# Kernel tuning notes

Hardware: AMD Instinct MI355X
Metric: run time of the kernel (lower is better)

The kernel has to match this reference:

```python
import jax, jax.numpy as jnp
import numpy as np

EPS = 1e-5  # nn.LayerNorm default eps
N_LAYERS, N, D_IN, H, D_OUT, NH = 4, 2048, 512, 1024, 256, 16


def setup_inputs() -> dict:
    key = jax.random.key(0)
    ks = jax.random.split(key, 8)
    s = lambda k, shape: (jax.random.normal(k, shape, jnp.float32) * 0.02)
    return {
        "x": jax.random.normal(ks[0], (N, D_IN), jnp.float32),
        "W1": s(ks[1], (H, D_IN)), "b1": jnp.zeros((H,), jnp.float32),
        # per-layer MHA params, stacked on a leading layer axis
        "Wqkv": s(ks[2], (N_LAYERS, 3 * H, H)), "bqkv": jnp.zeros((N_LAYERS, 3 * H), jnp.float32),
        "Wo": s(ks[3], (N_LAYERS, H, H)), "bo": jnp.zeros((N_LAYERS, H), jnp.float32),
        "ln_g": jnp.ones((N_LAYERS, H), jnp.float32), "ln_b": jnp.zeros((N_LAYERS, H), jnp.float32),
        "W2": s(ks[4], (D_OUT, H)), "b2": jnp.zeros((D_OUT,), jnp.float32),
        "g_out": jnp.ones((D_OUT,), jnp.float32), "b_out": jnp.zeros((D_OUT,), jnp.float32),
        "num_heads": NH,
    }


def layer_norm(x, g, b):
    m = jnp.mean(x, axis=-1, keepdims=True)
    v = jnp.mean(jnp.square(x - m), axis=-1, keepdims=True)
    return (x - m) * jax.lax.rsqrt(v + EPS) * g + b


def mha(x, Wqkv, bqkv, Wo, bo, nh):
    # x: [N, H]; attention is over the N axis (torch MHA with batch_first=False, batch=1)
    n, h = x.shape
    hd = h // nh
    qkv = x @ Wqkv.T + bqkv                      # [N, 3H]
    q, k, v = jnp.split(qkv, 3, axis=-1)
    q = q.reshape(n, nh, hd).transpose(1, 0, 2)  # [nh, N, hd]
    k = k.reshape(n, nh, hd).transpose(1, 0, 2)
    v = v.reshape(n, nh, hd).transpose(1, 0, 2)
    scale = jnp.float32(1.0 / np.sqrt(hd))
    scores = jnp.einsum('hnd,hmd->hnm', q, k) * scale  # [nh, N, N]
    attn = jax.nn.softmax(scores, axis=-1)
    out = jnp.einsum('hnm,hmd->hnd', attn, v)          # [nh, N, hd]
    out = out.transpose(1, 0, 2).reshape(n, h)
    return out @ Wo.T + bo


def reference(x, W1, b1, Wqkv, bqkv, Wo, bo, ln_g, ln_b, W2, b2, g_out, b_out, num_heads):
    h = jax.nn.relu(x @ W1.T + b1)  # dropout is identity in eval mode
    for i in range(Wqkv.shape[0]):
        a = mha(h, Wqkv[i], bqkv[i], Wo[i], bo[i], num_heads)
        h = layer_norm(a + h, ln_g[i], ln_b[i])
    y = jax.nn.relu(h @ W2.T + b2)
    return layer_norm(y, g_out, b_out)
```

## Files before the change

### kernel.cpp

```cpp
#include <hip/hip_runtime.h>

typedef __attribute__((ext_vector_type(8))) short short8;
typedef __attribute__((ext_vector_type(4))) float f32x4;
typedef __attribute__((ext_vector_type(16))) float f32x16;
typedef __attribute__((ext_vector_type(4))) float float4v;
typedef __attribute__((ext_vector_type(4))) unsigned short ushort4v;
typedef __attribute__((ext_vector_type(4))) unsigned int uint4v;
typedef __attribute__((ext_vector_type(2))) unsigned int uint2v;

#define MFMA16(a, b, c) __builtin_amdgcn_mfma_f32_16x16x32_bf16((a), (b), (c), 0, 0, 0)
#define MFMA32(a, b, c) __builtin_amdgcn_mfma_f32_32x32x16_bf16((a), (b), (c), 0, 0, 0)
#define GLOAD_LDS16(g, s)                                                         \
  __builtin_amdgcn_global_load_lds((const __attribute__((address_space(1))) void*)(g), \
                                   (__attribute__((address_space(3))) void*)(s), 16, 0, 0)
#define EXP2(x) __builtin_amdgcn_exp2f(x)

__device__ __forceinline__ unsigned short f2bf(float f) {
  unsigned u = __builtin_bit_cast(unsigned, f);
  u += 0x7fffu + ((u >> 16) & 1u);
  return (unsigned short)(u >> 16);
}

__device__ __forceinline__ unsigned cvtpk(float lo, float hi) {
  unsigned r;
  asm("v_cvt_pk_bf16_f32 %0, %1, %2" : "=v"(r) : "v"(lo), "v"(hi));
  return r;
}

__device__ __forceinline__ void swap32(unsigned& a, unsigned& b) {
  asm volatile("v_permlane32_swap_b32 %0, %1" : "+v"(a), "+v"(b));
}

__device__ __forceinline__ float bflo(unsigned u) {
  return __builtin_bit_cast(float, u << 16);
}
__device__ __forceinline__ float bfhi(unsigned u) {
  return __builtin_bit_cast(float, u & 0xffff0000u);
}

struct CvtArgs {
  const float* s[5];
  unsigned short* d[5];
  int off[6];
};

__global__ __launch_bounds__(256) void cvt_multi(CvtArgs a, int ntot4) {
  int i4 = blockIdx.x * 256 + threadIdx.x;
  const int stride = gridDim.x * 256;
  for (; i4 < ntot4; i4 += stride) {
    const int idx = i4 * 4;
    int s = 0;
#pragma unroll
    for (int k = 0; k < 4; ++k) s += (idx >= a.off[k + 1]) ? 1 : 0;
    const int local = idx - a.off[s];
    float4v v = *(const float4v*)(a.s[s] + local);
    ushort4v o;
    o.x = f2bf(v.x); o.y = f2bf(v.y); o.z = f2bf(v.z); o.w = f2bf(v.w);
    *(ushort4v*)(a.d[s] + local) = o;
  }
}

template <int BM, int BN, bool RELU, bool RES, bool OUTF, bool OUTB, bool OUTT>
__global__ __launch_bounds__(256) void gemm_bt(const unsigned short* __restrict__ A,
                                               const unsigned short* __restrict__ B,
                                               const float* __restrict__ bias,
                                               const float* __restrict__ res,
                                               float* __restrict__ outF,
                                               unsigned short* __restrict__ outB,
                                               unsigned short* __restrict__ outT,
                                               int tcol0, int ldt,
                                               int M, int N, int K) {
  __shared__ __align__(16) unsigned short As[2][BM * 32];
  __shared__ __align__(16) unsigned short Bs[2][BN * 32];
  constexpr int MI = BM / 32, MJ = BN / 32, CA = BM / 64, CB = BN / 64;
  const int tid = threadIdx.x;
  const int w = tid >> 6, lane = tid & 63;
  const int l15 = lane & 15, l4 = lane >> 4;

  const int nwg = gridDim.x;
  const int wg = (blockIdx.x & 7) * (nwg >> 3) + (blockIdx.x >> 3);
  const int nbx = N / BN;
  const int rowBase = (wg / nbx) * BM;
  const int colBase = (wg % nbx) * BN;
  const int wm = w >> 1, wn = w & 1;

  f32x4 acc[MI][MJ] = {};

  auto stage = [&](int buf, int k0) {
#pragma unroll
    for (int i = 0; i < CA; ++i) {
      const int c = i * 256 + tid;
      GLOAD_LDS16(A + (size_t)(rowBase + (c >> 2)) * K + k0 + ((c & 3) << 3),
                  As[buf] + i * 2048 + w * 512);
    }
#pragma unroll
    for (int i = 0; i < CB; ++i) {
      const int c = i * 256 + tid;
      GLOAD_LDS16(B + (size_t)(colBase + (c >> 2)) * K + k0 + ((c & 3) << 3),
                  Bs[buf] + i * 2048 + w * 512);
    }
  };

  stage(0, 0);
  __syncthreads();

  int p = 0;
  for (int k0 = 0; k0 < K; k0 += 32) {
    if (k0 + 32 < K) stage(p ^ 1, k0 + 32);

    short8 af[MI], bf[MJ];
#pragma unroll
    for (int f = 0; f < MI; ++f)
      af[f] = *(const short8*)(As[p] + (wm * (BM / 2) + f * 16 + l15) * 32 + l4 * 8);
#pragma unroll
    for (int f = 0; f < MJ; ++f)
      bf[f] = *(const short8*)(Bs[p] + (wn * (BN / 2) + f * 16 + l15) * 32 + l4 * 8);
#pragma unroll
    for (int i = 0; i < MI; ++i)
#pragma unroll
      for (int j = 0; j < MJ; ++j)
        acc[i][j] = MFMA16(af[i], bf[j], acc[i][j]);

    __syncthreads();
    p ^= 1;
  }

#pragma unroll
  for (int i = 0; i < MI; ++i) {
    const int row0 = rowBase + wm * (BM / 2) + i * 16 + l4 * 4;
#pragma unroll
    for (int j = 0; j < MJ; ++j) {
      const int col = colBase + wn * (BN / 2) + j * 16 + l15;
      const float bv = bias[col];
      float vv[4];
#pragma unroll
      for (int e = 0; e < 4; ++e) {
        float v = acc[i][j][e] + bv;
        if constexpr (RELU) v = fmaxf(v, 0.f);
        if constexpr (RES) v += res[(size_t)(row0 + e) * N + col];
        vv[e] = v;
        if constexpr (OUTF) outF[(size_t)(row0 + e) * N + col] = v;
        if constexpr (OUTB) outB[(size_t)(row0 + e) * N + col] = f2bf(v);
      }
      if constexpr (OUTT) {
        if (col >= tcol0) {
          ushort4v t;
          t.x = f2bf(vv[0]); t.y = f2bf(vv[1]); t.z = f2bf(vv[2]); t.w = f2bf(vv[3]);
          *(ushort4v*)(outT + (size_t)(col - tcol0) * ldt + row0) = t;
        }
      }
    }
  }
}

__global__ __launch_bounds__(256, 3) void flash_attn4(const unsigned short* __restrict__ qkv,
                                                      const unsigned short* __restrict__ vt,
                                                      unsigned short* __restrict__ Op0,
                                                      unsigned short* __restrict__ OpR,
                                                      float* __restrict__ Ml,
                                                      float* __restrict__ Ll,
                                                      int Nseq) {
  __shared__ __align__(16) unsigned short Ks[2][64 * 64];
  __shared__ __align__(16) unsigned short Vs[2][64 * 64];
  const int tid = threadIdx.x, w = tid >> 6, lane = tid & 63;
  const int l31 = lane & 31, l2h = lane >> 5, l7 = l31 & 7;
  const float CSC = 0.18033688011112042f;

  const int b = blockIdx.x;
  const int head = (b & 7) * 2 + ((b >> 3) & 1);
  const int s = (b >> 4) & 3;
  const int qb = b >> 6;
  const int q0w = qb * 128 + w * 32;

  const unsigned short* Qp = qkv + head * 64;
  const unsigned short* Kp = qkv + 1024 + head * 64;
  const unsigned short* Vtp = vt + (size_t)head * 64 * Nseq;

  short8 qf[4];
#pragma unroll
  for (int ka = 0; ka < 4; ++ka)
    qf[ka] = *(const short8*)(Qp + (size_t)(q0w + l31) * 3072 + ka * 16 + l2h * 8);

  f32x16 OT0 = {}, OT1 = {};
  float m = -1e30f, ls = 0.f;

  const int sr = tid >> 3, su = tid & 7;
  const int sOffA = sr * 64 + ((su ^ (sr & 7)) * 8);
  const int sOffB = sOffA + 32 * 64;

  const int kt0 = s * (Nseq >> 2);
  const int NIT = Nseq >> 8;

  short8 k0 = *(const short8*)(Kp + (size_t)(kt0 + sr) * 3072 + su * 8);
  short8 k1 = *(const short8*)(Kp + (size_t)(kt0 + sr + 32) * 3072 + su * 8);
  short8 v0 = *(const short8*)(Vtp + (size_t)sr * Nseq + kt0 + su * 8);
  short8 v1 = *(const short8*)(Vtp + (size_t)(sr + 32) * Nseq + kt0 + su * 8);
  *(short8*)(Ks[0] + sOffA) = k0;
  *(short8*)(Ks[0] + sOffB) = k1;
  *(short8*)(Vs[0] + sOffA) = v0;
  *(short8*)(Vs[0] + sOffB) = v1;
  __syncthreads();

  int p = 0;
  for (int it = 0; it < NIT; ++it) {
    const bool more = (it + 1) < NIT;
    if (more) {
      const int ktn = kt0 + (it + 1) * 64;
      k0 = *(const short8*)(Kp + (size_t)(ktn + sr) * 3072 + su * 8);
      k1 = *(const short8*)(Kp + (size_t)(ktn + sr + 32) * 3072 + su * 8);
      v0 = *(const short8*)(Vtp + (size_t)sr * Nseq + ktn + su * 8);
      v1 = *(const short8*)(Vtp + (size_t)(sr + 32) * Nseq + ktn + su * 8);
    }
    const unsigned short* KS = Ks[p];
    const unsigned short* VS = Vs[p];

    f32x16 S0 = {}, S1 = {};
    __builtin_amdgcn_s_setprio(1);
#pragma unroll
    for (int ka = 0; ka < 4; ++ka) {
      const int un = ((ka * 2 + l2h) ^ l7) * 8;
      const short8 a0 = *(const short8*)(KS + l31 * 64 + un);
      const short8 a1 = *(const short8*)(KS + (32 + l31) * 64 + un);
      S0 = MFMA32(a0, qf[ka], S0);
      S1 = MFMA32(a1, qf[ka], S1);
    }
    __builtin_amdgcn_s_setprio(0);

    float pm = S0[0];
#pragma unroll
    for (int r = 1; r < 16; ++r) pm = fmaxf(pm, S0[r]);
#pragma unroll
    for (int r = 0; r < 16; ++r) pm = fmaxf(pm, S1[r]);
    pm = fmaxf(pm, __shfl_xor(pm, 32));
    pm *= CSC;

    if (__any(pm > m + 8.f)) {
      const float mn = fmaxf(m, pm);
      const float fac = EXP2(m - mn);
      m = mn;
      ls *= fac;
#pragma unroll
      for (int r = 0; r < 16; ++r) { OT0[r] *= fac; OT1[r] *= fac; }
    }

    float rs = 0.f;
    unsigned W0[4][2], W1[4][2];
#pragma unroll
    for (int g = 0; g < 4; ++g) {
      const float a0 = EXP2(fmaf(S0[4 * g + 0], CSC, -m));
      const float a1 = EXP2(fmaf(S0[4 * g + 1], CSC, -m));
      const float a2 = EXP2(fmaf(S0[4 * g + 2], CSC, -m));
      const float a3 = EXP2(fmaf(S0[4 * g + 3], CSC, -m));
      const float b0 = EXP2(fmaf(S1[4 * g + 0], CSC, -m));
      const float b1 = EXP2(fmaf(S1[4 * g + 1], CSC, -m));
      const float b2 = EXP2(fmaf(S1[4 * g + 2], CSC, -m));
      const float b3 = EXP2(fmaf(S1[4 * g + 3], CSC, -m));
      rs += ((a0 + a1) + (a2 + a3)) + ((b0 + b1) + (b2 + b3));
      W0[g][0] = cvtpk(a0, a1); W0[g][1] = cvtpk(a2, a3);
      W1[g][0] = cvtpk(b0, b1); W1[g][1] = cvtpk(b2, b3);
    }
    rs += __shfl_xor(rs, 32);
    ls += rs;

    short8 pf[2][2];
#pragma unroll
    for (int ka = 0; ka < 2; ++ka) {
      {
        unsigned x0 = W0[2 * ka][0], y0 = W0[2 * ka + 1][0];
        unsigned x1 = W0[2 * ka][1], y1 = W0[2 * ka + 1][1];
        swap32(x0, y0);
        swap32(x1, y1);
        uint4v u = {x0, x1, y0, y1};
        pf[0][ka] = __builtin_bit_cast(short8, u);
      }
      {
        unsigned x0 = W1[2 * ka][0], y0 = W1[2 * ka + 1][0];
        unsigned x1 = W1[2 * ka][1], y1 = W1[2 * ka + 1][1];
        swap32(x0, y0);
        swap32(x1, y1);
        uint4v u = {x0, x1, y0, y1};
        pf[1][ka] = __builtin_bit_cast(short8, u);
      }
    }

    __builtin_amdgcn_s_setprio(1);
#pragma unroll
    for (int sub = 0; sub < 2; ++sub)
#pragma unroll
      for (int ka = 0; ka < 2; ++ka) {
        const int un = ((sub * 4 + ka * 2 + l2h) ^ l7) * 8;
        const short8 va0 = *(const short8*)(VS + l31 * 64 + un);
        const short8 va1 = *(const short8*)(VS + (32 + l31) * 64 + un);
        OT0 = MFMA32(va0, pf[sub][ka], OT0);
        OT1 = MFMA32(va1, pf[sub][ka], OT1);
      }
    __builtin_amdgcn_s_setprio(0);

    if (more) {
      unsigned short* Kn = Ks[p ^ 1];
      unsigned short* Vn = Vs[p ^ 1];
      *(short8*)(Kn + sOffA) = k0;
      *(short8*)(Kn + sOffB) = k1;
      *(short8*)(Vn + sOffA) = v0;
      *(short8*)(Vn + sOffB) = v1;
    }
    __syncthreads();
    p ^= 1;
  }

  unsigned short* Ob = (s == 0) ? Op0 : (OpR + (size_t)(s - 1) * Nseq * 1024);
  const int q = q0w + l31;
#pragma unroll
  for (int g = 0; g < 4; ++g) {
    const int d0 = 8 * g + 4 * l2h;
    uint2v t0 = {cvtpk(OT0[4 * g], OT0[4 * g + 1]), cvtpk(OT0[4 * g + 2], OT0[4 * g + 3])};
    uint2v t1 = {cvtpk(OT1[4 * g], OT1[4 * g + 1]), cvtpk(OT1[4 * g + 2], OT1[4 * g + 3])};
    *(uint2v*)(Ob + (size_t)q * 1024 + head * 64 + d0) = t0;
    *(uint2v*)(Ob + (size_t)q * 1024 + head * 64 + 32 + d0) = t1;
  }
  if (l2h == 0) {
    Ml[(size_t)(s * 16 + head) * Nseq + q] = m;
    Ll[(size_t)(s * 16 + head) * Nseq + q] = ls;
  }
}

__global__ __launch_bounds__(256) void attn_combine4(const unsigned short* __restrict__ Op0,
                                                     const unsigned short* __restrict__ OpR,
                                                     const float* __restrict__ Ml,
                                                     const float* __restrict__ Ll,
                                                     unsigned short* __restrict__ out, int Nseq) {
  const int t = blockIdx.x * 256 + threadIdx.x;
  const int q = t >> 8, c4 = (t & 255) * 4;
  const int head = c4 >> 6;
  float mm[4], lv[4];
  float M = -1e30f;
#pragma unroll
  for (int s = 0; s < 4; ++s) {
    mm[s] = Ml[(size_t)(s * 16 + head) * Nseq + q];
    lv[s] = Ll[(size_t)(s * 16 + head) * Nseq + q];
    M = fmaxf(M, mm[s]);
  }
  float denom = 0.f;
  float4v acc = {0.f, 0.f, 0.f, 0.f};
#pragma unroll
  for (int s = 0; s < 4; ++s) {
    const float ww = EXP2(mm[s] - M);
    denom += lv[s] * ww;
    const unsigned short* Ob = (s == 0) ? Op0 : (OpR + (size_t)(s - 1) * Nseq * 1024);
    uint2v o = *(const uint2v*)(Ob + (size_t)q * 1024 + c4);
    acc.x += bflo(o.x) * ww;
    acc.y += bfhi(o.x) * ww;
    acc.z += bflo(o.y) * ww;
    acc.w += bfhi(o.y) * ww;
  }
  const float inv = 1.f / denom;
  ushort4v r;
  r.x = f2bf(acc.x * inv);
  r.y = f2bf(acc.y * inv);
  r.z = f2bf(acc.z * inv);
  r.w = f2bf(acc.w * inv);
  *(ushort4v*)(out + (size_t)q * 1024 + c4) = r;
}

template <int D>
__global__ __launch_bounds__(256) void ln_rows(const float* __restrict__ src,
                                               const float* __restrict__ gw,
                                               const float* __restrict__ bw,
                                               float* __restrict__ outF,
                                               unsigned short* __restrict__ outB) {
  __shared__ float red[4];
  const int row = blockIdx.x;
  const int tid = threadIdx.x, w = tid >> 6;
  constexpr int PT = D / 256;
  const float* r = src + (size_t)row * D;
  float v[PT];
  float s = 0.f;
#pragma unroll
  for (int i = 0; i < PT; ++i) { v[i] = r[tid + i * 256]; s += v[i]; }
#pragma unroll
  for (int off = 32; off; off >>= 1) s += __shfl_down(s, off);
  if ((tid & 63) == 0) red[w] = s;
  __syncthreads();
  const float mean = (red[0] + red[1] + red[2] + red[3]) / D;
  __syncthreads();
  float q = 0.f;
#pragma unroll
  for (int i = 0; i < PT; ++i) { const float d = v[i] - mean; q += d * d; }
#pragma unroll
  for (int off = 32; off; off >>= 1) q += __shfl_down(q, off);
  if ((tid & 63) == 0) red[w] = q;
  __syncthreads();
  const float rstd = rsqrtf((red[0] + red[1] + red[2] + red[3]) / D + 1e-5f);
#pragma unroll
  for (int i = 0; i < PT; ++i) {
    const int c = tid + i * 256;
    const float o = (v[i] - mean) * rstd * gw[c] + bw[c];
    outF[(size_t)row * D + c] = o;
    if (outB) outB[(size_t)row * D + c] = f2bf(o);
  }
}

extern "C" void kernel_launch(void* const* d_in, const int* in_sizes, int n_in,
                              void* d_out, int out_size, void* d_ws, size_t ws_size,
                              hipStream_t stream) {
  const int N = 2048, D_IN = 512, H = 1024, D_OUT = 256, NL = 4;
  const float* x    = (const float*)d_in[0];
  const float* W1   = (const float*)d_in[1];
  const float* b1   = (const float*)d_in[2];
  const float* Wqkv = (const float*)d_in[3];
  const float* bqkv = (const float*)d_in[4];
  const float* Wo   = (const float*)d_in[5];
  const float* bo   = (const float*)d_in[6];
  const float* lng  = (const float*)d_in[7];
  const float* lnb  = (const float*)d_in[8];
  const float* W2   = (const float*)d_in[9];
  const float* b2   = (const float*)d_in[10];
  const float* gout = (const float*)d_in[11];
  const float* bout = (const float*)d_in[12];
  float* out = (float*)d_out;

  char* ws = (char*)d_ws;
  auto alloc = [&](size_t bytes) -> char* {
    char* p = ws;
    ws += (bytes + 255) & ~(size_t)255;
    return p;
  };
  unsigned short* xb    = (unsigned short*)alloc((size_t)N * D_IN * 2);
  unsigned short* W1b   = (unsigned short*)alloc((size_t)H * D_IN * 2);
  unsigned short* Wqkvb = (unsigned short*)alloc((size_t)NL * 3 * H * H * 2);
  unsigned short* Wob   = (unsigned short*)alloc((size_t)NL * H * H * 2);
  unsigned short* W2b   = (unsigned short*)alloc((size_t)D_OUT * H * 2);
  unsigned short* hb    = (unsigned short*)alloc((size_t)N * H * 2);
  unsigned short* qkvb  = (unsigned short*)alloc((size_t)N * 3 * H * 2);
  unsigned short* aob   = (unsigned short*)alloc((size_t)N * H * 2);
  unsigned short* vtg   = (unsigned short*)alloc((size_t)H * N * 2);
  unsigned short* opb0  = (unsigned short*)alloc((size_t)N * H * 2);
  unsigned short* opbR  = (unsigned short*)alloc((size_t)3 * N * H * 2);
  float* hf  = (float*)alloc((size_t)N * H * 4);
  float* af  = (float*)alloc((size_t)N * H * 4);
  float* ml  = (float*)alloc((size_t)4 * 16 * N * 4);
  float* ll  = (float*)alloc((size_t)4 * 16 * N * 4);
  float* yf  = (float*)alloc((size_t)N * D_OUT * 4);

  CvtArgs ca;
  ca.s[0] = x;    ca.d[0] = xb;
  ca.s[1] = W1;   ca.d[1] = W1b;
  ca.s[2] = Wqkv; ca.d[2] = Wqkvb;
  ca.s[3] = Wo;   ca.d[3] = Wob;
  ca.s[4] = W2;   ca.d[4] = W2b;
  const int n0 = N * D_IN, n1 = H * D_IN, n2 = NL * 3 * H * H, n3 = NL * H * H, n4 = D_OUT * H;
  ca.off[0] = 0;
  ca.off[1] = n0;
  ca.off[2] = n0 + n1;
  ca.off[3] = n0 + n1 + n2;
  ca.off[4] = n0 + n1 + n2 + n3;
  ca.off[5] = n0 + n1 + n2 + n3 + n4;
  const int ntot4 = ca.off[5] / 4;
  cvt_multi<<<2048, 256, 0, stream>>>(ca, ntot4);

  gemm_bt<128, 64, true, false, true, true, false><<<(N / 128) * (H / 64), 256, 0, stream>>>(
      xb, W1b, b1, nullptr, hf, hb, nullptr, 0, 0, N, H, D_IN);

  for (int l = 0; l < NL; ++l) {
    gemm_bt<128, 128, false, false, false, true, true><<<(N / 128) * (3 * H / 128), 256, 0, stream>>>(
        hb, Wqkvb + (size_t)l * 3 * H * H, bqkv + (size_t)l * 3 * H, nullptr, nullptr, qkvb,
        vtg, 2 * H, N, N, 3 * H, H);
    flash_attn4<<<1024, 256, 0, stream>>>(qkvb, vtg, opb0, opbR, ml, ll, N);
    attn_combine4<<<(N * H / 4) / 256, 256, 0, stream>>>(opb0, opbR, ml, ll, aob, N);
    gemm_bt<128, 64, false, true, true, false, false><<<(N / 128) * (H / 64), 256, 0, stream>>>(
        aob, Wob + (size_t)l * H * H, bo + (size_t)l * H, hf, af, nullptr, nullptr, 0, 0,
        N, H, H);
    ln_rows<1024><<<N, 256, 0, stream>>>(af, lng + (size_t)l * H, lnb + (size_t)l * H, hf, hb);
  }

  gemm_bt<64, 64, true, false, true, false, false><<<(N / 64) * (D_OUT / 64), 256, 0, stream>>>(
      hb, W2b, b2, nullptr, yf, nullptr, nullptr, 0, 0, N, D_OUT, H);
  ln_rows<256><<<N, 256, 0, stream>>>(yf, gout, bout, out, nullptr);
}
```

Before: 417.0 us.

## Fuse attention split-combine into flash kernel and use bf16 residual stream

The separate attention combine kernel is removed. The last of the four split-K flash blocks for each (head, query block) now merges the partial outputs itself, using an atomic counter and threadfence to detect that it is last. The fp32 residual copy of h is dropped, so the output-projection GEMM reads the bf16 h as its residual and layer norm writes only bf16. The W1 and Wo GEMMs move to 64x64 tiles. This saves one launch per layer and fp32 residual traffic, at the cost of residual precision, a tail of serialized combine work in the last blocks, and a memset for the counters.

```diff
diff --git a/kernel.cpp b/kernel.cpp
--- a/kernel.cpp
+++ b/kernel.cpp
@@ -37,6 +37,9 @@
 __device__ __forceinline__ float bfhi(unsigned u) {
   return __builtin_bit_cast(float, u & 0xffff0000u);
 }
+__device__ __forceinline__ float bf2f(unsigned short u) {
+  return __builtin_bit_cast(float, (unsigned)u << 16);
+}
 
 struct CvtArgs {
   const float* s[5];
@@ -64,7 +67,7 @@
 __global__ __launch_bounds__(256) void gemm_bt(const unsigned short* __restrict__ A,
                                                const unsigned short* __restrict__ B,
                                                const float* __restrict__ bias,
-                                               const float* __restrict__ res,
+                                               const unsigned short* __restrict__ resB,
                                                float* __restrict__ outF,
                                                unsigned short* __restrict__ outB,
                                                unsigned short* __restrict__ outT,
@@ -137,7 +140,7 @@
       for (int e = 0; e < 4; ++e) {
         float v = acc[i][j][e] + bv;
         if constexpr (RELU) v = fmaxf(v, 0.f);
-        if constexpr (RES) v += res[(size_t)(row0 + e) * N + col];
+        if constexpr (RES) v += bf2f(resB[(size_t)(row0 + e) * N + col]);
         vv[e] = v;
         if constexpr (OUTF) outF[(size_t)(row0 + e) * N + col] = v;
         if constexpr (OUTB) outB[(size_t)(row0 + e) * N + col] = f2bf(v);
@@ -153,12 +156,14 @@
   }
 }
 
-__global__ __launch_bounds__(256, 3) void flash_attn4(const unsigned short* __restrict__ qkv,
+__global__ __launch_bounds__(256, 3) void flash_attn5(const unsigned short* __restrict__ qkv,
                                                       const unsigned short* __restrict__ vt,
                                                       unsigned short* __restrict__ Op0,
                                                       unsigned short* __restrict__ OpR,
                                                       float* __restrict__ Ml,
                                                       float* __restrict__ Ll,
+                                                      unsigned short* __restrict__ aout,
+                                                      int* __restrict__ cnt,
                                                       int Nseq) {
   __shared__ __align__(16) unsigned short Ks[2][64 * 64];
   __shared__ __align__(16) unsigned short Vs[2][64 * 64];
@@ -322,47 +327,53 @@
     Ml[(size_t)(s * 16 + head) * Nseq + q] = m;
     Ll[(size_t)(s * 16 + head) * Nseq + q] = ls;
   }
-}
-
-__global__ __launch_bounds__(256) void attn_combine4(const unsigned short* __restrict__ Op0,
-                                                     const unsigned short* __restrict__ OpR,
-                                                     const float* __restrict__ Ml,
-                                                     const float* __restrict__ Ll,
-                                                     unsigned short* __restrict__ out, int Nseq) {
-  const int t = blockIdx.x * 256 + threadIdx.x;
-  const int q = t >> 8, c4 = (t & 255) * 4;
-  const int head = c4 >> 6;
-  float mm[4], lv[4];
-  float M = -1e30f;
-#pragma unroll
-  for (int s = 0; s < 4; ++s) {
-    mm[s] = Ml[(size_t)(s * 16 + head) * Nseq + q];
-    lv[s] = Ll[(size_t)(s * 16 + head) * Nseq + q];
-    M = fmaxf(M, mm[s]);
-  }
-  float denom = 0.f;
-  float4v acc = {0.f, 0.f, 0.f, 0.f};
-#pragma unroll
-  for (int s = 0; s < 4; ++s) {
-    const float ww = EXP2(mm[s] - M);
-    denom += lv[s] * ww;
-    const unsigned short* Ob = (s == 0) ? Op0 : (OpR + (size_t)(s - 1) * Nseq * 1024);
-    uint2v o = *(const uint2v*)(Ob + (size_t)q * 1024 + c4);
-    acc.x += bflo(o.x) * ww;
-    acc.y += bfhi(o.x) * ww;
-    acc.z += bflo(o.y) * ww;
-    acc.w += bfhi(o.y) * ww;
-  }
-  const float inv = 1.f / denom;
-  ushort4v r;
-  r.x = f2bf(acc.x * inv);
-  r.y = f2bf(acc.y * inv);
-  r.z = f2bf(acc.z * inv);
-  r.w = f2bf(acc.w * inv);
-  *(ushort4v*)(out + (size_t)q * 1024 + c4) = r;
-}
-
-template <int D>
+
+  __threadfence();
+  __shared__ int lastFlag;
+  if (tid == 0) {
+    const int old = atomicAdd(cnt + head * 16 + qb, 1);
+    lastFlag = (old == 3);
+  }
+  __syncthreads();
+  if (lastFlag) {
+    __threadfence();
+    const int q0base = qb * 128;
+    for (int i = tid; i < 128 * 16; i += 256) {
+      const int qr = q0base + (i >> 4);
+      const int c4 = head * 64 + (i & 15) * 4;
+      float mm[4], lv[4];
+      float M = -1e30f;
+#pragma unroll
+      for (int s2 = 0; s2 < 4; ++s2) {
+        mm[s2] = Ml[(size_t)(s2 * 16 + head) * Nseq + qr];
+        lv[s2] = Ll[(size_t)(s2 * 16 + head) * Nseq + qr];
+        M = fmaxf(M, mm[s2]);
+      }
+      float denom = 0.f;
+      float4v acc = {0.f, 0.f, 0.f, 0.f};
+#pragma unroll
+      for (int s2 = 0; s2 < 4; ++s2) {
+        const float ww = EXP2(mm[s2] - M);
+        denom += lv[s2] * ww;
+        const unsigned short* Ob2 = (s2 == 0) ? Op0 : (OpR + (size_t)(s2 - 1) * Nseq * 1024);
+        uint2v o = *(const uint2v*)(Ob2 + (size_t)qr * 1024 + c4);
+        acc.x += bflo(o.x) * ww;
+        acc.y += bfhi(o.x) * ww;
+        acc.z += bflo(o.y) * ww;
+        acc.w += bfhi(o.y) * ww;
+      }
+      const float inv = 1.f / denom;
+      ushort4v r;
+      r.x = f2bf(acc.x * inv);
+      r.y = f2bf(acc.y * inv);
+      r.z = f2bf(acc.z * inv);
+      r.w = f2bf(acc.w * inv);
+      *(ushort4v*)(aout + (size_t)qr * 1024 + c4) = r;
+    }
+  }
+}
+
+template <int D, bool WF, bool WB>
 __global__ __launch_bounds__(256) void ln_rows(const float* __restrict__ src,
                                                const float* __restrict__ gw,
                                                const float* __restrict__ bw,
@@ -395,8 +406,8 @@
   for (int i = 0; i < PT; ++i) {
     const int c = tid + i * 256;
     const float o = (v[i] - mean) * rstd * gw[c] + bw[c];
-    outF[(size_t)row * D + c] = o;
-    if (outB) outB[(size_t)row * D + c] = f2bf(o);
+    if constexpr (WF) outF[(size_t)row * D + c] = o;
+    if constexpr (WB) outB[(size_t)row * D + c] = f2bf(o);
   }
 }
 
@@ -436,11 +447,13 @@
   unsigned short* vtg   = (unsigned short*)alloc((size_t)H * N * 2);
   unsigned short* opb0  = (unsigned short*)alloc((size_t)N * H * 2);
   unsigned short* opbR  = (unsigned short*)alloc((size_t)3 * N * H * 2);
-  float* hf  = (float*)alloc((size_t)N * H * 4);
+  int*   cnt = (int*)alloc((size_t)NL * 256 * 4);
   float* af  = (float*)alloc((size_t)N * H * 4);
   float* ml  = (float*)alloc((size_t)4 * 16 * N * 4);
   float* ll  = (float*)alloc((size_t)4 * 16 * N * 4);
   float* yf  = (float*)alloc((size_t)N * D_OUT * 4);
+
+  hipMemsetAsync(cnt, 0, (size_t)NL * 256 * 4, stream);
 
   CvtArgs ca;
   ca.s[0] = x;    ca.d[0] = xb;
@@ -458,22 +471,23 @@
   const int ntot4 = ca.off[5] / 4;
   cvt_multi<<<2048, 256, 0, stream>>>(ca, ntot4);
 
-  gemm_bt<128, 64, true, false, true, true, false><<<(N / 128) * (H / 64), 256, 0, stream>>>(
-      xb, W1b, b1, nullptr, hf, hb, nullptr, 0, 0, N, H, D_IN);
+  gemm_bt<64, 64, true, false, false, true, false><<<(N / 64) * (H / 64), 256, 0, stream>>>(
+      xb, W1b, b1, nullptr, nullptr, hb, nullptr, 0, 0, N, H, D_IN);
 
   for (int l = 0; l < NL; ++l) {
     gemm_bt<128, 128, false, false, false, true, true><<<(N / 128) * (3 * H / 128), 256, 0, stream>>>(
         hb, Wqkvb + (size_t)l * 3 * H * H, bqkv + (size_t)l * 3 * H, nullptr, nullptr, qkvb,
         vtg, 2 * H, N, N, 3 * H, H);
-    flash_attn4<<<1024, 256, 0, stream>>>(qkvb, vtg, opb0, opbR, ml, ll, N);
-    attn_combine4<<<(N * H / 4) / 256, 256, 0, stream>>>(opb0, opbR, ml, ll, aob, N);
-    gemm_bt<128, 64, false, true, true, false, false><<<(N / 128) * (H / 64), 256, 0, stream>>>(
-        aob, Wob + (size_t)l * H * H, bo + (size_t)l * H, hf, af, nullptr, nullptr, 0, 0,
+    flash_attn5<<<1024, 256, 0, stream>>>(qkvb, vtg, opb0, opbR, ml, ll, aob,
+                                          cnt + l * 256, N);
+    gemm_bt<64, 64, false, true, true, false, false><<<(N / 64) * (H / 64), 256, 0, stream>>>(
+        aob, Wob + (size_t)l * H * H, bo + (size_t)l * H, hb, af, nullptr, nullptr, 0, 0,
         N, H, H);
-    ln_rows<1024><<<N, 256, 0, stream>>>(af, lng + (size_t)l * H, lnb + (size_t)l * H, hf, hb);
+    ln_rows<1024, false, true><<<N, 256, 0, stream>>>(af, lng + (size_t)l * H,
+                                                      lnb + (size_t)l * H, nullptr, hb);
   }
 
   gemm_bt<64, 64, true, false, true, false, false><<<(N / 64) * (D_OUT / 64), 256, 0, stream>>>(
       hb, W2b, b2, nullptr, yf, nullptr, nullptr, 0, 0, N, D_OUT, H);
-  ln_rows<256><<<N, 256, 0, stream>>>(yf, gout, bout, out, nullptr);
-}
+  ln_rows<256, true, false><<<N, 256, 0, stream>>>(yf, gout, bout, out, nullptr);
+}
```

New measurement: 1.046 ms. +150.9%, slower.
